# Performance work log

Measured on AMD Instinct MI355X. Metric: run time of the kernel, lower is better.

The kernel has to match this reference:

```python
import jax, jax.numpy as jnp
import numpy as np

B, N, D = 8, 4096, 512
K = 1228  # int(4096 * 0.3)
N_CH = 2


def setup_inputs() -> dict:
    key = jax.random.key(0)
    ks = jax.random.split(key, 6)
    return {
        "agents_states": jax.random.normal(ks[0], (B, N, D), jnp.float32),
        "net": jax.random.normal(ks[1], (N_CH, N, N), jnp.float32) * (1.0 / np.sqrt(N)),
        "gate_w": jax.random.normal(ks[2], (N_CH, D, 2 * D), jnp.float32) * 0.02,
        "gate_b": jnp.zeros((N_CH, D), jnp.float32),
        "cand_w": jax.random.normal(ks[3], (N_CH, D, D), jnp.float32) * 0.02,
        "cand_b": jnp.zeros((N_CH, D), jnp.float32),
        "ln_g": jnp.ones((N_CH, D), jnp.float32),
        "ln_b": jnp.zeros((N_CH, D), jnp.float32),
        "channel_mix": jnp.ones((N_CH,), jnp.float32) / N_CH,
        "k": K,
    }


def _layer_norm(h, g, b, eps=1e-5):
    mu = h.mean(-1, keepdims=True)
    var = jnp.mean((h - mu) ** 2, axis=-1, keepdims=True)
    return (h - mu) * jax.lax.rsqrt(var + eps) * g + b


def _channel(x, net, gw, gb, cw, cb, lg, lb):
    # fixed-graph message passing: [N,N] @ [B,N,D]
    interaction = jnp.einsum('mn,bnd->bmd', net, x)
    candidate = jax.nn.gelu(interaction @ cw.T + cb, approximate=False)
    gate = jax.nn.sigmoid(jnp.concatenate([x, interaction], axis=-1) @ gw.T + gb)
    return _layer_norm(gate * candidate + (1.0 - gate) * x, lg, lb)


def reference(agents_states, net, gate_w, gate_b, cand_w, cand_b, ln_g, ln_b, channel_mix, k):
    w = jax.nn.softmax(channel_mix, axis=0)
    out = jnp.zeros_like(agents_states)
    for c in range(net.shape[0]):  # fixed small channel count
        out = out + w[c] * _channel(agents_states, net[c], gate_w[c], gate_b[c],
                                    cand_w[c], cand_b[c], ln_g[c], ln_b[c])
    # sparse top-k activation over agents
    energy = jnp.linalg.norm(out, axis=-1)               # [B, N]
    _, top_idx = jax.lax.top_k(energy, k)                # [B, k]
    mask = jnp.zeros_like(energy).at[jnp.arange(energy.shape[0])[:, None], top_idx].set(1.0)
    mask = mask * (out.shape[1] / k)
    return out * mask[..., None]
```

## Files before the change

kernel.cpp:

```cpp
#include <hip/hip_runtime.h>
#include <hip/hip_bf16.h>
#include <math.h>

#define BB 8
#define NN 4096
#define DD 512
#define SLAB 2048
#define SROWS (BB * SLAB)

typedef short bf16x8 __attribute__((ext_vector_type(8)));
typedef float f32x4 __attribute__((ext_vector_type(4)));

#define AS1 __attribute__((address_space(1)))
#define AS3 __attribute__((address_space(3)))

__device__ __forceinline__ void gload_lds16(const void* g, void* l) {
    __builtin_amdgcn_global_load_lds((const AS1 unsigned int*)g,
                                     (AS3 unsigned int*)l, 16, 0, 0);
}

__device__ __forceinline__ void split_bf16(float v, unsigned short& h, unsigned short& l) {
    __hip_bfloat16 bh = __float2bfloat16(v);
    float hf = __bfloat162float(bh);
    __hip_bfloat16 bl = __float2bfloat16(v - hf);
    h = *reinterpret_cast<unsigned short*>(&bh);
    l = *reinterpret_cast<unsigned short*>(&bl);
}

__global__ __launch_bounds__(256)
void conv_split(const float* __restrict__ src, unsigned short* __restrict__ hi,
                unsigned short* __restrict__ lo)
{
    const size_t i = (size_t)blockIdx.x * 256 + threadIdx.x;
    float4 v = ((const float4*)src)[i];
    ushort4 h, l;
    split_bf16(v.x, h.x, l.x);
    split_bf16(v.y, h.y, l.y);
    split_bf16(v.z, h.z, l.z);
    split_bf16(v.w, h.w, l.w);
    ((ushort4*)hi)[i] = h;
    ((ushort4*)lo)[i] = l;
}

__global__ __launch_bounds__(256)
void conv_w3(const float* __restrict__ cw, const float* __restrict__ gw,
             unsigned short* __restrict__ cwh, unsigned short* __restrict__ cwl,
             unsigned short* __restrict__ gxh, unsigned short* __restrict__ gxl,
             unsigned short* __restrict__ gih, unsigned short* __restrict__ gil)
{
    const int blk = blockIdx.x;
    const int i = (blk & 255) * 256 + threadIdx.x;
    const int n = i >> 7, kq = (i & 127) * 4;
    const float* src;
    unsigned short *oh, *ol;
    if (blk < 256)      { src = cw + (size_t)n * 512 + kq;        oh = cwh; ol = cwl; }
    else if (blk < 512) { src = gw + (size_t)n * 1024 + kq;       oh = gxh; ol = gxl; }
    else                { src = gw + (size_t)n * 1024 + 512 + kq; oh = gih; ol = gil; }
    float4 v = *(const float4*)src;
    ushort4 h, l;
    split_bf16(v.x, h.x, l.x);
    split_bf16(v.y, h.y, l.y);
    split_bf16(v.z, h.z, l.z);
    split_bf16(v.w, h.w, l.w);
    *(ushort4*)(oh + (size_t)n * 512 + kq) = h;
    *(ushort4*)(ol + (size_t)n * 512 + kq) = l;
}

__global__ __launch_bounds__(256)
void conv_xs(const float* __restrict__ x, int nbase,
             unsigned short* __restrict__ hi, unsigned short* __restrict__ lo)
{
    const size_t i = (size_t)blockIdx.x * 256 + threadIdx.x;
    const int r = (int)(i >> 7), kq = (int)(i & 127) * 4;
    const int b = r >> 11, ii = r & (SLAB - 1);
    float4 v = *(const float4*)(x + ((size_t)(b << 12) + nbase + ii) * DD + kq);
    ushort4 h, l;
    split_bf16(v.x, h.x, l.x);
    split_bf16(v.y, h.y, l.y);
    split_bf16(v.z, h.z, l.z);
    split_bf16(v.w, h.w, l.w);
    *(ushort4*)(hi + (size_t)r * DD + kq) = h;
    *(ushort4*)(lo + (size_t)r * DD + kq) = l;
}

__global__ __launch_bounds__(256)
void conv_xT(const float* __restrict__ x, unsigned short* __restrict__ th,
             unsigned short* __restrict__ tl)
{
    __shared__ unsigned short Th[64][65];
    __shared__ unsigned short Tl[64][65];
    const int n0 = blockIdx.x * 64, d0 = blockIdx.y * 64, b = blockIdx.z;
    const int t = threadIdx.x;
    const int r = t >> 4, c4 = (t & 15) * 4;
#pragma unroll
    for (int i = 0; i < 4; ++i) {
        int row = r + i * 16;
        float4 v = *(const float4*)(x + ((size_t)b * NN + n0 + row) * DD + d0 + c4);
        split_bf16(v.x, Th[row][c4 + 0], Tl[row][c4 + 0]);
        split_bf16(v.y, Th[row][c4 + 1], Tl[row][c4 + 1]);
        split_bf16(v.z, Th[row][c4 + 2], Tl[row][c4 + 2]);
        split_bf16(v.w, Th[row][c4 + 3], Tl[row][c4 + 3]);
    }
    __syncthreads();
    const int od = t >> 2;
    const int on0 = (t & 3) * 16;
    unsigned short hb[16], lb[16];
#pragma unroll
    for (int j = 0; j < 16; ++j) { hb[j] = Th[on0 + j][od]; lb[j] = Tl[on0 + j][od]; }
    const size_t obase = ((size_t)b * DD + d0 + od) * (size_t)NN + n0 + on0;
#pragma unroll
    for (int q = 0; q < 4; ++q) {
        ushort4 hv = {hb[q * 4 + 0], hb[q * 4 + 1], hb[q * 4 + 2], hb[q * 4 + 3]};
        ushort4 lv = {lb[q * 4 + 0], lb[q * 4 + 1], lb[q * 4 + 2], lb[q * 4 + 3]};
        *(ushort4*)(th + obase + q * 4) = hv;
        *(ushort4*)(tl + obase + q * 4) = lv;
    }
}

__global__ __launch_bounds__(256, 2)
void gemm_big(const unsigned short* __restrict__ Ah, const unsigned short* __restrict__ Al,
              const unsigned short* __restrict__ Bh, const unsigned short* __restrict__ Bl,
              unsigned short* __restrict__ Ch, unsigned short* __restrict__ Cl)
{
    __shared__ alignas(16) unsigned short sAh[128 * 32];
    __shared__ alignas(16) unsigned short sAl[128 * 32];
    __shared__ alignas(16) unsigned short sBh[128 * 32];
    __shared__ alignas(16) unsigned short sBl[128 * 32];

    const int tid = threadIdx.x;
    const int lane = tid & 63;
    const int w = tid >> 6;

    const int lin = blockIdx.x + (blockIdx.y << 2) + (blockIdx.z << 5);
    const int swz = (lin & 7) * 64 + (lin >> 3);
    const int n0 = (swz & 3) * 128;
    const int b  = (swz >> 2) & 7;
    const int m0 = (swz >> 5) * 128;

    Bh += (size_t)b * DD * NN;
    Bl += (size_t)b * DD * NN;

    const int c0 = w * 2, c1 = c0 + 1;
    const int u2 = lane >> 2;
    const int sst = (u2 + (u2 >> 2)) & 3;
    const int kc = (lane & 3) ^ sst;
    const size_t gA0 = (size_t)(m0 + c0 * 16 + u2) * NN + kc * 8;
    const size_t gA1 = (size_t)(m0 + c1 * 16 + u2) * NN + kc * 8;
    const size_t gB0 = (size_t)(n0 + c0 * 16 + u2) * NN + kc * 8;
    const size_t gB1 = (size_t)(n0 + c1 * 16 + u2) * NN + kc * 8;
    unsigned short* lAh0 = sAh + c0 * 512; unsigned short* lAh1 = sAh + c1 * 512;
    unsigned short* lAl0 = sAl + c0 * 512; unsigned short* lAl1 = sAl + c1 * 512;
    unsigned short* lBh0 = sBh + c0 * 512; unsigned short* lBh1 = sBh + c1 * 512;
    unsigned short* lBl0 = sBl + c0 * 512; unsigned short* lBl1 = sBl + c1 * 512;

    const int wm = (w & 1) * 64, wn = (w >> 1) * 64;
    const int fr = lane & 15;
    const int sf = (fr + (fr >> 2)) & 3;
    const int fslot = ((lane >> 4) ^ sf) * 16;
    int offA[4], offB[4];
#pragma unroll
    for (int i = 0; i < 4; ++i) {
        offA[i] = (wm + i * 16 + fr) * 64 + fslot;
        offB[i] = (wn + i * 16 + fr) * 64 + fslot;
    }

    f32x4 acc[4][4] = {};

    for (int kt = 0; kt < NN; kt += 32) {
        __syncthreads();
        gload_lds16(Ah + gA0 + kt, lAh0);
        gload_lds16(Ah + gA1 + kt, lAh1);
        gload_lds16(Al + gA0 + kt, lAl0);
        gload_lds16(Al + gA1 + kt, lAl1);
        gload_lds16(Bh + gB0 + kt, lBh0);
        gload_lds16(Bh + gB1 + kt, lBh1);
        gload_lds16(Bl + gB0 + kt, lBl0);
        gload_lds16(Bl + gB1 + kt, lBl1);
        asm volatile("s_waitcnt vmcnt(0)" ::: "memory");
        __syncthreads();

        bf16x8 ah[4], al[4], bh[4], bl[4];
#pragma unroll
        for (int i = 0; i < 4; ++i) {
            ah[i] = *(const bf16x8*)((const char*)sAh + offA[i]);
            al[i] = *(const bf16x8*)((const char*)sAl + offA[i]);
            bh[i] = *(const bf16x8*)((const char*)sBh + offB[i]);
            bl[i] = *(const bf16x8*)((const char*)sBl + offB[i]);
        }
#pragma unroll
        for (int mi = 0; mi < 4; ++mi)
#pragma unroll
            for (int ni = 0; ni < 4; ++ni) {
                acc[mi][ni] = __builtin_amdgcn_mfma_f32_16x16x32_bf16(al[mi], bh[ni], acc[mi][ni], 0, 0, 0);
                acc[mi][ni] = __builtin_amdgcn_mfma_f32_16x16x32_bf16(ah[mi], bl[ni], acc[mi][ni], 0, 0, 0);
                acc[mi][ni] = __builtin_amdgcn_mfma_f32_16x16x32_bf16(ah[mi], bh[ni], acc[mi][ni], 0, 0, 0);
            }
    }

    const int erow = (lane >> 4) * 4;
#pragma unroll
    for (int mi = 0; mi < 4; ++mi)
#pragma unroll
        for (int ni = 0; ni < 4; ++ni) {
            const int r0 = m0 + wm + mi * 16 + erow;
            const int col = n0 + wn + ni * 16 + fr;
#pragma unroll
            for (int r = 0; r < 4; ++r) {
                unsigned short h, l;
                split_bf16(acc[mi][ni][r], h, l);
                const size_t idx = ((size_t)b * SLAB + r0 + r) * DD + col;
                Ch[idx] = h;
                Cl[idx] = l;
            }
        }
}

__global__ __launch_bounds__(256, 2)
void gemm_small(const unsigned short* __restrict__ Ah, const unsigned short* __restrict__ Al,
                const unsigned short* __restrict__ Bh, const unsigned short* __restrict__ Bl,
                const float* __restrict__ bias, float* __restrict__ C, int accum)
{
    __shared__ alignas(16) unsigned short sAh[128 * 32];
    __shared__ alignas(16) unsigned short sAl[128 * 32];
    __shared__ alignas(16) unsigned short sBh[128 * 32];
    __shared__ alignas(16) unsigned short sBl[128 * 32];

    const int tid = threadIdx.x;
    const int lane = tid & 63;
    const int w = tid >> 6;

    const int lin = blockIdx.x + (blockIdx.y << 2);
    const int swz = (lin & 7) * 64 + (lin >> 3);
    const int n0 = (swz & 3) * 128;
    const int m0 = (swz >> 2) * 128;

    const int c0 = w * 2, c1 = c0 + 1;
    const int u2 = lane >> 2;
    const int sst = (u2 + (u2 >> 2)) & 3;
    const int kc = (lane & 3) ^ sst;
    const size_t gA0 = (size_t)(m0 + c0 * 16 + u2) * DD + kc * 8;
    const size_t gA1 = (size_t)(m0 + c1 * 16 + u2) * DD + kc * 8;
    const size_t gB0 = (size_t)(n0 + c0 * 16 + u2) * DD + kc * 8;
    const size_t gB1 = (size_t)(n0 + c1 * 16 + u2) * DD + kc * 8;
    unsigned short* lAh0 = sAh + c0 * 512; unsigned short* lAh1 = sAh + c1 * 512;
    unsigned short* lAl0 = sAl + c0 * 512; unsigned short* lAl1 = sAl + c1 * 512;
    unsigned short* lBh0 = sBh + c0 * 512; unsigned short* lBh1 = sBh + c1 * 512;
    unsigned short* lBl0 = sBl + c0 * 512; unsigned short* lBl1 = sBl + c1 * 512;

    const int wm = (w & 1) * 64, wn = (w >> 1) * 64;
    const int fr = lane & 15;
    const int sf = (fr + (fr >> 2)) & 3;
    const int fslot = ((lane >> 4) ^ sf) * 16;
    int offA[4], offB[4];
#pragma unroll
    for (int i = 0; i < 4; ++i) {
        offA[i] = (wm + i * 16 + fr) * 64 + fslot;
        offB[i] = (wn + i * 16 + fr) * 64 + fslot;
    }

    f32x4 acc[4][4] = {};

    for (int kt = 0; kt < DD; kt += 32) {
        __syncthreads();
        gload_lds16(Ah + gA0 + kt, lAh0);
        gload_lds16(Ah + gA1 + kt, lAh1);
        gload_lds16(Al + gA0 + kt, lAl0);
        gload_lds16(Al + gA1 + kt, lAl1);
        gload_lds16(Bh + gB0 + kt, lBh0);
        gload_lds16(Bh + gB1 + kt, lBh1);
        gload_lds16(Bl + gB0 + kt, lBl0);
        gload_lds16(Bl + gB1 + kt, lBl1);
        asm volatile("s_waitcnt vmcnt(0)" ::: "memory");
        __syncthreads();

        bf16x8 ah[4], al[4], bh[4], bl[4];
#pragma unroll
        for (int i = 0; i < 4; ++i) {
            ah[i] = *(const bf16x8*)((const char*)sAh + offA[i]);
            al[i] = *(const bf16x8*)((const char*)sAl + offA[i]);
            bh[i] = *(const bf16x8*)((const char*)sBh + offB[i]);
            bl[i] = *(const bf16x8*)((const char*)sBl + offB[i]);
        }
#pragma unroll
        for (int mi = 0; mi < 4; ++mi)
#pragma unroll
            for (int ni = 0; ni < 4; ++ni) {
                acc[mi][ni] = __builtin_amdgcn_mfma_f32_16x16x32_bf16(al[mi], bh[ni], acc[mi][ni], 0, 0, 0);
                acc[mi][ni] = __builtin_amdgcn_mfma_f32_16x16x32_bf16(ah[mi], bl[ni], acc[mi][ni], 0, 0, 0);
                acc[mi][ni] = __builtin_amdgcn_mfma_f32_16x16x32_bf16(ah[mi], bh[ni], acc[mi][ni], 0, 0, 0);
            }
    }

    const int erow = (lane >> 4) * 4;
#pragma unroll
    for (int mi = 0; mi < 4; ++mi)
#pragma unroll
        for (int ni = 0; ni < 4; ++ni) {
            const int r0 = m0 + wm + mi * 16 + erow;
            const int col = n0 + wn + ni * 16 + fr;
            const float bv = bias ? bias[col] : 0.0f;
#pragma unroll
            for (int r = 0; r < 4; ++r) {
                const size_t idx = (size_t)(r0 + r) * DD + col;
                float v = acc[mi][ni][r] + bv;
                if (accum) v += C[idx];
                C[idx] = v;
            }
        }
}

__global__ __launch_bounds__(256, 2)
void gemm_small_dual(const unsigned short* __restrict__ Ah, const unsigned short* __restrict__ Al,
                     const unsigned short* __restrict__ Gh, const unsigned short* __restrict__ Gl,
                     const unsigned short* __restrict__ Wh, const unsigned short* __restrict__ Wl,
                     const float* __restrict__ cbias, float* __restrict__ gatep,
                     float* __restrict__ candp)
{
    __shared__ alignas(16) unsigned short sAh[128 * 32];
    __shared__ alignas(16) unsigned short sAl[128 * 32];
    __shared__ alignas(16) unsigned short sGh[128 * 32];
    __shared__ alignas(16) unsigned short sGl[128 * 32];
    __shared__ alignas(16) unsigned short sWh[128 * 32];
    __shared__ alignas(16) unsigned short sWl[128 * 32];

    const int tid = threadIdx.x;
    const int lane = tid & 63;
    const int w = tid >> 6;

    const int lin = blockIdx.x + (blockIdx.y << 2);
    const int swz = (lin & 7) * 64 + (lin >> 3);
    const int n0 = (swz & 3) * 128;
    const int m0 = (swz >> 2) * 128;

    const int c0 = w * 2, c1 = c0 + 1;
    const int u2 = lane >> 2;
    const int sst = (u2 + (u2 >> 2)) & 3;
    const int kc = (lane & 3) ^ sst;
    const size_t gA0 = (size_t)(m0 + c0 * 16 + u2) * DD + kc * 8;
    const size_t gA1 = (size_t)(m0 + c1 * 16 + u2) * DD + kc * 8;
    const size_t gB0 = (size_t)(n0 + c0 * 16 + u2) * DD + kc * 8;
    const size_t gB1 = (size_t)(n0 + c1 * 16 + u2) * DD + kc * 8;

    const int wm = (w & 1) * 64, wn = (w >> 1) * 64;
    const int fr = lane & 15;
    const int sf = (fr + (fr >> 2)) & 3;
    const int fslot = ((lane >> 4) ^ sf) * 16;
    int offA[4], offB[4];
#pragma unroll
    for (int i = 0; i < 4; ++i) {
        offA[i] = (wm + i * 16 + fr) * 64 + fslot;
        offB[i] = (wn + i * 16 + fr) * 64 + fslot;
    }

    f32x4 accG[4][4] = {};
    f32x4 accC[4][4] = {};

    for (int kt = 0; kt < DD; kt += 32) {
        __syncthreads();
        gload_lds16(Ah + gA0 + kt, sAh + c0 * 512);
        gload_lds16(Ah + gA1 + kt, sAh + c1 * 512);
        gload_lds16(Al + gA0 + kt, sAl + c0 * 512);
        gload_lds16(Al + gA1 + kt, sAl + c1 * 512);
        gload_lds16(Gh + gB0 + kt, sGh + c0 * 512);
        gload_lds16(Gh + gB1 + kt, sGh + c1 * 512);
        gload_lds16(Gl + gB0 + kt, sGl + c0 * 512);
        gload_lds16(Gl + gB1 + kt, sGl + c1 * 512);
        gload_lds16(Wh + gB0 + kt, sWh + c0 * 512);
        gload_lds16(Wh + gB1 + kt, sWh + c1 * 512);
        gload_lds16(Wl + gB0 + kt, sWl + c0 * 512);
        gload_lds16(Wl + gB1 + kt, sWl + c1 * 512);
        asm volatile("s_waitcnt vmcnt(0)" ::: "memory");
        __syncthreads();

        bf16x8 ah[4], al[4], bh[4], bl[4];
#pragma unroll
        for (int i = 0; i < 4; ++i) {
            ah[i] = *(const bf16x8*)((const char*)sAh + offA[i]);
            al[i] = *(const bf16x8*)((const char*)sAl + offA[i]);
        }
#pragma unroll
        for (int i = 0; i < 4; ++i) {
            bh[i] = *(const bf16x8*)((const char*)sGh + offB[i]);
            bl[i] = *(const bf16x8*)((const char*)sGl + offB[i]);
        }
#pragma unroll
        for (int mi = 0; mi < 4; ++mi)
#pragma unroll
            for (int ni = 0; ni < 4; ++ni) {
                accG[mi][ni] = __builtin_amdgcn_mfma_f32_16x16x32_bf16(al[mi], bh[ni], accG[mi][ni], 0, 0, 0);
                accG[mi][ni] = __builtin_amdgcn_mfma_f32_16x16x32_bf16(ah[mi], bl[ni], accG[mi][ni], 0, 0, 0);
                accG[mi][ni] = __builtin_amdgcn_mfma_f32_16x16x32_bf16(ah[mi], bh[ni], accG[mi][ni], 0, 0, 0);
            }
#pragma unroll
        for (int i = 0; i < 4; ++i) {
            bh[i] = *(const bf16x8*)((const char*)sWh + offB[i]);
            bl[i] = *(const bf16x8*)((const char*)sWl + offB[i]);
        }
#pragma unroll
        for (int mi = 0; mi < 4; ++mi)
#pragma unroll
            for (int ni = 0; ni < 4; ++ni) {
                accC[mi][ni] = __builtin_amdgcn_mfma_f32_16x16x32_bf16(al[mi], bh[ni], accC[mi][ni], 0, 0, 0);
                accC[mi][ni] = __builtin_amdgcn_mfma_f32_16x16x32_bf16(ah[mi], bl[ni], accC[mi][ni], 0, 0, 0);
                accC[mi][ni] = __builtin_amdgcn_mfma_f32_16x16x32_bf16(ah[mi], bh[ni], accC[mi][ni], 0, 0, 0);
            }
    }

    const int erow = (lane >> 4) * 4;
#pragma unroll
    for (int mi = 0; mi < 4; ++mi)
#pragma unroll
        for (int ni = 0; ni < 4; ++ni) {
            const int r0 = m0 + wm + mi * 16 + erow;
            const int col = n0 + wn + ni * 16 + fr;
            const float cb = cbias[col];
#pragma unroll
            for (int r = 0; r < 4; ++r) {
                const size_t idx = (size_t)(r0 + r) * DD + col;
                gatep[idx] += accG[mi][ni][r];
                candp[idx] = accC[mi][ni][r] + cb;
            }
        }
}

__global__ __launch_bounds__(128)
void pw_slab(const float* __restrict__ x, const float* __restrict__ gp_,
             const float* __restrict__ cp_, const float* __restrict__ lg,
             const float* __restrict__ lb, const float* __restrict__ cmix,
             int c, int nbase, float* __restrict__ out, float* __restrict__ energy)
{
    __shared__ float sm[4];
    const int rloc = blockIdx.x;
    const int b = rloc >> 11, ii = rloc & (SLAB - 1);
    const int grow = (b << 12) + nbase + ii;
    const int tid = threadIdx.x;
    const size_t lbase = (size_t)rloc * DD + tid * 4;
    const size_t gbase = (size_t)grow * DD + tid * 4;

    float4 g4 = *(const float4*)(gp_ + lbase);
    float4 c4 = *(const float4*)(cp_ + lbase);
    float4 x4 = *(const float4*)(x + gbase);
    float gv[4] = {g4.x, g4.y, g4.z, g4.w};
    float cv[4] = {c4.x, c4.y, c4.z, c4.w};
    float xv[4] = {x4.x, x4.y, x4.z, x4.w};
    float h[4];
#pragma unroll
    for (int j = 0; j < 4; ++j) {
        float gate = 1.0f / (1.0f + expf(-gv[j]));
        float cand = 0.5f * cv[j] * (1.0f + erff(cv[j] * 0.70710678118654752440f));
        h[j] = gate * cand + (1.0f - gate) * xv[j];
    }

    const int lane = tid & 63, wid = tid >> 6;
    float s = h[0] + h[1] + h[2] + h[3];
#pragma unroll
    for (int off = 32; off > 0; off >>= 1) s += __shfl_xor(s, off, 64);
    if (lane == 0) sm[wid] = s;
    __syncthreads();
    float mu = (sm[0] + sm[1]) * (1.0f / 512.0f);
    float vs = 0.0f;
#pragma unroll
    for (int j = 0; j < 4; ++j) { float d = h[j] - mu; vs += d * d; }
#pragma unroll
    for (int off = 32; off > 0; off >>= 1) vs += __shfl_xor(vs, off, 64);
    if (lane == 0) sm[2 + wid] = vs;
    __syncthreads();
    float var = (sm[2] + sm[3]) * (1.0f / 512.0f);
    float rstd = 1.0f / sqrtf(var + 1e-5f);

    float m0 = cmix[0], m1 = cmix[1];
    float mx = fmaxf(m0, m1);
    float e0 = expf(m0 - mx), e1 = expf(m1 - mx);
    float wgt = ((c == 0) ? e0 : e1) / (e0 + e1);

    const int dix = tid * 4;
    float4 lg4 = *(const float4*)(lg + dix);
    float4 lb4 = *(const float4*)(lb + dix);
    float lgv[4] = {lg4.x, lg4.y, lg4.z, lg4.w};
    float lbv[4] = {lb4.x, lb4.y, lb4.z, lb4.w};
    float ov[4];
    if (c == 0) {
#pragma unroll
        for (int j = 0; j < 4; ++j)
            ov[j] = wgt * ((h[j] - mu) * rstd * lgv[j] + lbv[j]);
    } else {
        float4 o4 = *(const float4*)(out + gbase);
        ov[0] = o4.x; ov[1] = o4.y; ov[2] = o4.z; ov[3] = o4.w;
#pragma unroll
        for (int j = 0; j < 4; ++j)
            ov[j] += wgt * ((h[j] - mu) * rstd * lgv[j] + lbv[j]);
    }
    float4 st = {ov[0], ov[1], ov[2], ov[3]};
    *(float4*)(out + gbase) = st;

    if (c == 1) {
        float s2 = ov[0] * ov[0] + ov[1] * ov[1] + ov[2] * ov[2] + ov[3] * ov[3];
#pragma unroll
        for (int off = 32; off > 0; off >>= 1) s2 += __shfl_xor(s2, off, 64);
        __syncthreads();
        if (lane == 0) sm[wid] = s2;
        __syncthreads();
        if (tid == 0) energy[grow] = sqrtf(sm[0] + sm[1]);
    }
}

__global__ __launch_bounds__(1024)
void topk_kernel(float* __restrict__ energy, const int* __restrict__ kptr)
{
    __shared__ unsigned keys[NN];
    __shared__ int hist[256];
    __shared__ int wsum[16];
    __shared__ unsigned sh_pfx;
    __shared__ int sh_need;

    const int b = blockIdx.x, tid = threadIdx.x;
    float* e = energy + (size_t)b * NN;
    for (int n = tid; n < NN; n += 1024) keys[n] = __float_as_uint(e[n]);
    const int K = *kptr;
    if (tid == 0) { sh_pfx = 0u; sh_need = K; }
    __syncthreads();

    for (int round = 0; round < 4; ++round) {
        const int shift = 24 - 8 * round;
        if (tid < 256) hist[tid] = 0;
        __syncthreads();
        const unsigned pfx = sh_pfx;
        const unsigned mhi = (round == 0) ? 0u : (0xFFFFFFFFu << (shift + 8));
        for (int n = tid; n < NN; n += 1024) {
            unsigned kv = keys[n];
            if ((kv & mhi) == pfx) atomicAdd(&hist[(kv >> shift) & 255], 1);
        }
        __syncthreads();
        if (tid == 0) {
            int need = sh_need;
            int d = 255;
            for (;; --d) {
                int cct = hist[d];
                if (need <= cct) break;
                need -= cct;
            }
            sh_pfx = pfx | ((unsigned)d << shift);
            sh_need = need;
        }
        __syncthreads();
    }

    const unsigned T = sh_pfx;
    const int need = sh_need;

    const int n0 = tid * 4;
    unsigned kv[4]; int eq[4]; int loc[4];
    int s = 0;
#pragma unroll
    for (int j = 0; j < 4; ++j) {
        kv[j] = keys[n0 + j];
        eq[j] = (kv[j] == T) ? 1 : 0;
        loc[j] = s; s += eq[j];
    }
    const int lane = tid & 63, wid = tid >> 6;
    int v = s;
#pragma unroll
    for (int off = 1; off < 64; off <<= 1) {
        int u = __shfl_up(v, off, 64);
        if (lane >= off) v += u;
    }
    if (lane == 63) wsum[wid] = v;
    __syncthreads();
    if (tid == 0) {
        int acc = 0;
        for (int w2 = 0; w2 < 16; ++w2) { int t = wsum[w2]; wsum[w2] = acc; acc += t; }
    }
    __syncthreads();
    const int base = wsum[wid] + (v - s);
    const float scale = (float)(4096.0 / (double)K);
#pragma unroll
    for (int j = 0; j < 4; ++j) {
        bool sel = (kv[j] > T) || (eq[j] && (base + loc[j]) < need);
        e[n0 + j] = sel ? scale : 0.0f;
    }
}

__global__ __launch_bounds__(128)
void mask_kernel(float* __restrict__ out, const float* __restrict__ mscale)
{
    const int row = blockIdx.x;
    const int tid = threadIdx.x;
    const size_t base = (size_t)row * DD + tid * 4;
    const float sc = mscale[row];
    float4 v = *(const float4*)(out + base);
    v.x *= sc; v.y *= sc; v.z *= sc; v.w *= sc;
    *(float4*)(out + base) = v;
}

extern "C" void kernel_launch(void* const* d_in, const int* in_sizes, int n_in,
                              void* d_out, int out_size, void* d_ws, size_t ws_size,
                              hipStream_t stream)
{
    const float* x      = (const float*)d_in[0];
    const float* net    = (const float*)d_in[1];
    const float* gate_w = (const float*)d_in[2];
    const float* gate_b = (const float*)d_in[3];
    const float* cand_w = (const float*)d_in[4];
    const float* cand_b = (const float*)d_in[5];
    const float* ln_g   = (const float*)d_in[6];
    const float* ln_b   = (const float*)d_in[7];
    const float* cmix   = (const float*)d_in[8];
    const int*   kptr   = (const int*)d_in[9];
    float* out = (float*)d_out;

    const size_t ROWS  = (size_t)BB * NN;
    const size_t PLANE = ROWS * DD;

    char* p = (char*)d_ws;
    unsigned short* xTh = (unsigned short*)p;             p += PLANE * 2;
    unsigned short* xTl = (unsigned short*)p;             p += PLANE * 2;
    char* slotN = p;                                      p += (size_t)SLAB * NN * 2 * 2;
    unsigned short* netsh = (unsigned short*)slotN;
    unsigned short* netsl = netsh + (size_t)SLAB * NN;
    unsigned short* cwh = (unsigned short*)slotN;
    unsigned short* cwl = cwh + 512 * 512;
    unsigned short* gxh = cwl + 512 * 512;
    unsigned short* gxl = gxh + 512 * 512;
    unsigned short* gih = gxl + 512 * 512;
    unsigned short* gil = gih + 512 * 512;
    unsigned short* inth = (unsigned short*)p;            p += (size_t)SROWS * DD * 2;
    unsigned short* intl = (unsigned short*)p;            p += (size_t)SROWS * DD * 2;
    char* slotX = p;                                      p += (size_t)SROWS * DD * 4;
    unsigned short* xsh = (unsigned short*)slotX;
    unsigned short* xsl = xsh + (size_t)SROWS * DD;
    float* candp = (float*)slotX;
    float* gatep = (float*)p;                             p += (size_t)SROWS * DD * 4;
    float* energy = (float*)p;

    conv_xT<<<dim3(NN / 64, DD / 64, BB), 256, 0, stream>>>(x, xTh, xTl);

    for (int c = 0; c < 2; ++c) {
        for (int s = 0; s < 2; ++s) {
            const int nbase = s * SLAB;
            conv_split<<<(SLAB * NN / 4) / 256, 256, 0, stream>>>(
                net + (size_t)c * NN * NN + (size_t)nbase * NN, netsh, netsl);
            gemm_big<<<dim3(DD / 128, BB, SLAB / 128), 256, 0, stream>>>(
                netsh, netsl, xTh, xTl, inth, intl);
            conv_w3<<<768, 256, 0, stream>>>(
                cand_w + (size_t)c * DD * DD, gate_w + (size_t)c * DD * 2 * DD,
                cwh, cwl, gxh, gxl, gih, gil);
            conv_xs<<<(SROWS * DD / 4) / 256, 256, 0, stream>>>(x, nbase, xsh, xsl);
            gemm_small<<<dim3(4, SROWS / 128), 256, 0, stream>>>(
                xsh, xsl, gxh, gxl, gate_b + (size_t)c * DD, gatep, 0);
            gemm_small_dual<<<dim3(4, SROWS / 128), 256, 0, stream>>>(
                inth, intl, gih, gil, cwh, cwl, cand_b + (size_t)c * DD, gatep, candp);
            pw_slab<<<SROWS, 128, 0, stream>>>(
                x, gatep, candp, ln_g + (size_t)c * DD, ln_b + (size_t)c * DD,
                cmix, c, nbase, out, energy);
        }
    }

    topk_kernel<<<BB, 1024, 0, stream>>>(energy, kptr);
    mask_kernel<<<(int)ROWS, 128, 0, stream>>>(out, energy);
}
```

Before: 1.690 ms.

## Triple-buffer gemm_big LDS loads with 256x128 tiles and 512 threads

Reworks the main interaction GEMM to use a three-stage LDS ring buffer: global-to-LDS loads for two tiles ahead are issued before compute, with partial vmcnt waits and a single barrier per k-step instead of two. The block tile grows to 256x128 with 8 waves, halving the block count and reducing B-operand reloads, and MFMA sections get raised wave priority. This aims to hide global memory latency behind the split-bf16 MFMA work, at the cost of much larger LDS usage (about 144KB per block), which may limit occupancy to one block per CU.

Result: slower. 1.822 ms (+7.8%).

```diff
diff --git a/kernel.cpp b/kernel.cpp
--- a/kernel.cpp
+++ b/kernel.cpp
@@ -117,43 +117,47 @@
     }
 }
 
-__global__ __launch_bounds__(256, 2)
+__global__ __launch_bounds__(512, 2)
 void gemm_big(const unsigned short* __restrict__ Ah, const unsigned short* __restrict__ Al,
               const unsigned short* __restrict__ Bh, const unsigned short* __restrict__ Bl,
               unsigned short* __restrict__ Ch, unsigned short* __restrict__ Cl)
 {
-    __shared__ alignas(16) unsigned short sAh[128 * 32];
-    __shared__ alignas(16) unsigned short sAl[128 * 32];
-    __shared__ alignas(16) unsigned short sBh[128 * 32];
-    __shared__ alignas(16) unsigned short sBl[128 * 32];
+    __shared__ alignas(16) unsigned short sA[3][2][256 * 32];
+    __shared__ alignas(16) unsigned short sB[3][2][128 * 32];
 
     const int tid = threadIdx.x;
     const int lane = tid & 63;
     const int w = tid >> 6;
 
     const int lin = blockIdx.x + (blockIdx.y << 2) + (blockIdx.z << 5);
-    const int swz = (lin & 7) * 64 + (lin >> 3);
+    const int swz = (lin & 7) * 32 + (lin >> 3);
     const int n0 = (swz & 3) * 128;
     const int b  = (swz >> 2) & 7;
-    const int m0 = (swz >> 5) * 128;
+    const int m0 = (swz >> 5) * 256;
 
     Bh += (size_t)b * DD * NN;
     Bl += (size_t)b * DD * NN;
 
-    const int c0 = w * 2, c1 = c0 + 1;
     const int u2 = lane >> 2;
     const int sst = (u2 + (u2 >> 2)) & 3;
     const int kc = (lane & 3) ^ sst;
-    const size_t gA0 = (size_t)(m0 + c0 * 16 + u2) * NN + kc * 8;
-    const size_t gA1 = (size_t)(m0 + c1 * 16 + u2) * NN + kc * 8;
-    const size_t gB0 = (size_t)(n0 + c0 * 16 + u2) * NN + kc * 8;
-    const size_t gB1 = (size_t)(n0 + c1 * 16 + u2) * NN + kc * 8;
-    unsigned short* lAh0 = sAh + c0 * 512; unsigned short* lAh1 = sAh + c1 * 512;
-    unsigned short* lAl0 = sAl + c0 * 512; unsigned short* lAl1 = sAl + c1 * 512;
-    unsigned short* lBh0 = sBh + c0 * 512; unsigned short* lBh1 = sBh + c1 * 512;
-    unsigned short* lBl0 = sBl + c0 * 512; unsigned short* lBl1 = sBl + c1 * 512;
-
-    const int wm = (w & 1) * 64, wn = (w >> 1) * 64;
+    const int cA0 = w * 2, cA1 = w * 2 + 1;
+    const int cB = w;
+    const size_t gA0 = (size_t)(m0 + cA0 * 16 + u2) * NN + kc * 8;
+    const size_t gA1 = (size_t)(m0 + cA1 * 16 + u2) * NN + kc * 8;
+    const size_t gB  = (size_t)(n0 + cB * 16 + u2) * NN + kc * 8;
+
+    auto stage = [&](int r, int koff) {
+        gload_lds16(Ah + gA0 + koff, sA[r][0] + cA0 * 512);
+        gload_lds16(Ah + gA1 + koff, sA[r][0] + cA1 * 512);
+        gload_lds16(Al + gA0 + koff, sA[r][1] + cA0 * 512);
+        gload_lds16(Al + gA1 + koff, sA[r][1] + cA1 * 512);
+        gload_lds16(Bh + gB + koff,  sB[r][0] + cB * 512);
+        gload_lds16(Bl + gB + koff,  sB[r][1] + cB * 512);
+    };
+
+    const int wm = (w & 3) * 64;
+    const int wn = (w >> 2) * 64;
     const int fr = lane & 15;
     const int sf = (fr + (fr >> 2)) & 3;
     const int fslot = ((lane >> 4) ^ sf) * 16;
@@ -166,27 +170,31 @@
 
     f32x4 acc[4][4] = {};
 
-    for (int kt = 0; kt < NN; kt += 32) {
-        __syncthreads();
-        gload_lds16(Ah + gA0 + kt, lAh0);
-        gload_lds16(Ah + gA1 + kt, lAh1);
-        gload_lds16(Al + gA0 + kt, lAl0);
-        gload_lds16(Al + gA1 + kt, lAl1);
-        gload_lds16(Bh + gB0 + kt, lBh0);
-        gload_lds16(Bh + gB1 + kt, lBh1);
-        gload_lds16(Bl + gB0 + kt, lBl0);
-        gload_lds16(Bl + gB1 + kt, lBl1);
-        asm volatile("s_waitcnt vmcnt(0)" ::: "memory");
-        __syncthreads();
+    stage(0, 0);
+    stage(1, 32);
+
+    for (int it = 0; it < NN / 32; ++it) {
+        const int kt = it * 32;
+        if (kt + 32 < NN) asm volatile("s_waitcnt vmcnt(6)" ::: "memory");
+        else              asm volatile("s_waitcnt vmcnt(0)" ::: "memory");
+        __builtin_amdgcn_s_barrier();
+        asm volatile("" ::: "memory");
+        if (kt + 64 < NN) stage((it + 2) % 3, kt + 64);
+
+        const unsigned short* pA = &sA[it % 3][0][0];
+        const unsigned short* pAl = &sA[it % 3][1][0];
+        const unsigned short* pB = &sB[it % 3][0][0];
+        const unsigned short* pBl = &sB[it % 3][1][0];
 
         bf16x8 ah[4], al[4], bh[4], bl[4];
 #pragma unroll
         for (int i = 0; i < 4; ++i) {
-            ah[i] = *(const bf16x8*)((const char*)sAh + offA[i]);
-            al[i] = *(const bf16x8*)((const char*)sAl + offA[i]);
-            bh[i] = *(const bf16x8*)((const char*)sBh + offB[i]);
-            bl[i] = *(const bf16x8*)((const char*)sBl + offB[i]);
-        }
+            ah[i] = *(const bf16x8*)((const char*)pA + offA[i]);
+            al[i] = *(const bf16x8*)((const char*)pAl + offA[i]);
+            bh[i] = *(const bf16x8*)((const char*)pB + offB[i]);
+            bl[i] = *(const bf16x8*)((const char*)pBl + offB[i]);
+        }
+        __builtin_amdgcn_s_setprio(1);
 #pragma unroll
         for (int mi = 0; mi < 4; ++mi)
 #pragma unroll
@@ -195,6 +203,7 @@
                 acc[mi][ni] = __builtin_amdgcn_mfma_f32_16x16x32_bf16(ah[mi], bl[ni], acc[mi][ni], 0, 0, 0);
                 acc[mi][ni] = __builtin_amdgcn_mfma_f32_16x16x32_bf16(ah[mi], bh[ni], acc[mi][ni], 0, 0, 0);
             }
+        __builtin_amdgcn_s_setprio(0);
     }
 
     const int erow = (lane >> 4) * 4;
@@ -639,7 +648,7 @@
             const int nbase = s * SLAB;
             conv_split<<<(SLAB * NN / 4) / 256, 256, 0, stream>>>(
                 net + (size_t)c * NN * NN + (size_t)nbase * NN, netsh, netsl);
-            gemm_big<<<dim3(DD / 128, BB, SLAB / 128), 256, 0, stream>>>(
+            gemm_big<<<dim3(4, 8, 8), 512, 0, stream>>>(
                 netsh, netsl, xTh, xTl, inth, intl);
             conv_w3<<<768, 256, 0, stream>>>(
                 cand_w + (size_t)c * DD * DD, gate_w + (size_t)c * DD * 2 * DD,
```
